# Kernel optimization log

Measured on AMD Instinct MI355X. Metric: run time of the kernel, lower is better.

Reference implementation:

```python
import jax, jax.numpy as jnp
import numpy as np
import math

D_MODEL = 1024
N_HEADS = 16
D_K = D_MODEL // N_HEADS
D_FF = 4096
B, T = 1, 4096
EPS = 1e-5


def _layer_norm(x, g, b):
    mu = jnp.mean(x, axis=-1, keepdims=True)
    var = jnp.mean(jnp.square(x - mu), axis=-1, keepdims=True)
    return (x - mu) * jax.lax.rsqrt(var + EPS) * g + b


def setup_inputs() -> dict:
    key = jax.random.key(0)
    ks = jax.random.split(key, 8)
    s = 0.02
    return {
        "x": jax.random.normal(ks[0], (B, T, D_MODEL), dtype=jnp.float32),
        "ln1_g": jnp.ones((D_MODEL,), jnp.float32),
        "ln1_b": jnp.zeros((D_MODEL,), jnp.float32),
        "w_qkv": jax.random.normal(ks[1], (3 * D_MODEL, D_MODEL), jnp.float32) * s,
        "b_qkv": jnp.zeros((3 * D_MODEL,), jnp.float32),
        "w_out": jax.random.normal(ks[2], (D_MODEL, D_MODEL), jnp.float32) * s,
        "b_out": jnp.zeros((D_MODEL,), jnp.float32),
        "ln2_g": jnp.ones((D_MODEL,), jnp.float32),
        "ln2_b": jnp.zeros((D_MODEL,), jnp.float32),
        "w1": jax.random.normal(ks[3], (D_FF, D_MODEL), jnp.float32) * s,
        "b1": jnp.zeros((D_FF,), jnp.float32),
        "w2": jax.random.normal(ks[4], (D_MODEL, D_FF), jnp.float32) * s,
        "b2": jnp.zeros((D_MODEL,), jnp.float32),
    }


def reference(x, ln1_g, ln1_b, w_qkv, b_qkv, w_out, b_out, ln2_g, ln2_b, w1, b1, w2, b2):
    Bx, Tx, C = x.shape
    # --- attention (pre-norm) ---
    h = _layer_norm(x, ln1_g, ln1_b)
    qkv = h @ w_qkv.T + b_qkv                      # [B,T,3C]
    q, k, v = jnp.split(qkv, 3, axis=-1)
    def heads(t):  # [B,T,C] -> [B,H,T,dk]
        return t.reshape(Bx, Tx, N_HEADS, D_K).transpose(0, 2, 1, 3)
    q, k, v = heads(q), heads(k), heads(v)
    scale = math.sqrt(D_K)
    scores = jnp.einsum("bhqd,bhkd->bhqk", q, k) / scale
    causal = jnp.triu(jnp.ones((Tx, Tx), dtype=bool), k=1)
    scores = jnp.where(causal[None, None], -jnp.inf, scores)
    attn_weights = jax.nn.softmax(scores, axis=-1)  # [B,H,T,T]
    out = jnp.einsum("bhqk,bhkd->bhqd", attn_weights, v)
    out = out.transpose(0, 2, 1, 3).reshape(Bx, Tx, C)
    attn_out = out @ w_out.T + b_out
    x = x + attn_out
    # --- FFN (pre-norm) ---
    h2 = _layer_norm(x, ln2_g, ln2_b)
    ff = jax.nn.gelu(h2 @ w1.T + b1, approximate=False) @ w2.T + b2
    x = x + ff
    return (x, attn_weights)
```

## Files before the change

kernel.cpp:

```cpp
#include <hip/hip_runtime.h>
#include <math.h>

typedef unsigned short u16;
typedef unsigned int u32;
typedef __attribute__((ext_vector_type(8))) short bf16x8;
typedef __attribute__((ext_vector_type(4))) float f32x4;

#define MFMA16(a, b, c) __builtin_amdgcn_mfma_f32_16x16x32_bf16((a), (b), (c), 0, 0, 0)

__device__ __forceinline__ u16 f2bf(float f) {
  u32 u = __float_as_uint(f);
  return (u16)((u + 0x7fffu + ((u >> 16) & 1u)) >> 16);
}

typedef const __attribute__((address_space(1))) u32* gas_t;
typedef __attribute__((address_space(3))) u32* las_t;
__device__ __forceinline__ void gl_lds16(const u16* g, u16* l) {
  __builtin_amdgcn_global_load_lds((gas_t)g, (las_t)l, 16, 0, 0);
}

__global__ __launch_bounds__(256) void cvt_bf16_kernel(const float* __restrict__ in,
                                                       u16* __restrict__ out, int n4) {
  int i = blockIdx.x * 256 + threadIdx.x;
  if (i >= n4) return;
  float4 v = ((const float4*)in)[i];
  ushort4 o;
  o.x = f2bf(v.x); o.y = f2bf(v.y); o.z = f2bf(v.z); o.w = f2bf(v.w);
  ((ushort4*)out)[i] = o;
}

__global__ __launch_bounds__(256) void ln_kernel(const float* __restrict__ x,
                                                 const float* __restrict__ g,
                                                 const float* __restrict__ b,
                                                 u16* __restrict__ out) {
  int row = blockIdx.x, tid = threadIdx.x;
  float4 v = ((const float4*)(x + (size_t)row * 1024))[tid];
  float s = v.x + v.y + v.z + v.w;
  float s2 = v.x * v.x + v.y * v.y + v.z * v.z + v.w * v.w;
  for (int off = 32; off; off >>= 1) { s += __shfl_xor(s, off); s2 += __shfl_xor(s2, off); }
  __shared__ float ps[4], ps2[4];
  int wave = tid >> 6;
  if ((tid & 63) == 0) { ps[wave] = s; ps2[wave] = s2; }
  __syncthreads();
  float fs = ps[0] + ps[1] + ps[2] + ps[3];
  float fs2 = ps2[0] + ps2[1] + ps2[2] + ps2[3];
  float mu = fs * (1.0f / 1024.0f);
  float var = fs2 * (1.0f / 1024.0f) - mu * mu;
  float rs = rsqrtf(var + 1e-5f);
  float4 gv = ((const float4*)g)[tid];
  float4 bv = ((const float4*)b)[tid];
  ushort4 o;
  o.x = f2bf((v.x - mu) * rs * gv.x + bv.x);
  o.y = f2bf((v.y - mu) * rs * gv.y + bv.y);
  o.z = f2bf((v.z - mu) * rs * gv.z + bv.z);
  o.w = f2bf((v.w - mu) * rs * gv.w + bv.w);
  ((ushort4*)(out + (size_t)row * 1024))[tid] = o;
}

__global__ __launch_bounds__(256) void vtrans_kernel(const u16* __restrict__ qkv,
                                                     u16* __restrict__ vt) {
  const int tt = blockIdx.x, h = blockIdx.y;
  __shared__ u16 tile[64 * 68];
  const int tid = threadIdx.x;
#pragma unroll
  for (int i = 0; i < 2; i++) {
    int c = i * 256 + tid;
    int trow = c >> 3, dc = c & 7;
    const u16* src = qkv + (size_t)(tt * 64 + trow) * 3072 + 2048 + h * 64 + dc * 8;
    uint4 v = *(const uint4*)src;
    *(uint2*)&tile[trow * 68 + dc * 8] = make_uint2(v.x, v.y);
    *(uint2*)&tile[trow * 68 + dc * 8 + 4] = make_uint2(v.z, v.w);
  }
  __syncthreads();
#pragma unroll
  for (int i = 0; i < 2; i++) {
    int c = i * 256 + tid;
    int d = c >> 3, tc = c & 7;
    ushort4 o0, o1;
    o0.x = tile[(tc * 8 + 0) * 68 + d]; o0.y = tile[(tc * 8 + 1) * 68 + d];
    o0.z = tile[(tc * 8 + 2) * 68 + d]; o0.w = tile[(tc * 8 + 3) * 68 + d];
    o1.x = tile[(tc * 8 + 4) * 68 + d]; o1.y = tile[(tc * 8 + 5) * 68 + d];
    o1.z = tile[(tc * 8 + 6) * 68 + d]; o1.w = tile[(tc * 8 + 7) * 68 + d];
    u16* dst = vt + (size_t)(h * 64 + d) * 4096 + tt * 64 + tc * 8;
    *(ushort4*)dst = o0;
    *(ushort4*)(dst + 4) = o1;
  }
}

template <int EPI>
__global__ __launch_bounds__(256, 2) void gemm_bf16(const u16* __restrict__ A,
                                                    const u16* __restrict__ B,
                                                    const float* __restrict__ bias,
                                                    const float* __restrict__ resid,
                                                    void* __restrict__ Cout,
                                                    int M, int N, int K) {
  __shared__ u16 As[128 * 32];
  __shared__ u16 Bs[128 * 32];
  const int tid = threadIdx.x, lane = tid & 63, wave = tid >> 6;
  const int wr = wave >> 1, wc = wave & 1;
  const int bm = blockIdx.y * 128, bn = blockIdx.x * 128;
  const int r = lane & 15, qd = lane >> 4;

  const u16 *ag[2], *bg[2];
  u16 *al[2], *bl[2];
#pragma unroll
  for (int i = 0; i < 2; i++) {
    int C0 = wave * 128 + i * 64;
    int sc = C0 + lane;
    int row = sc >> 2;
    int q = (sc & 3) ^ ((row >> 1) & 3);
    ag[i] = A + (size_t)(bm + row) * K + q * 8;
    al[i] = &As[C0 * 8];
    bg[i] = B + (size_t)(bn + row) * K + q * 8;
    bl[i] = &Bs[C0 * 8];
  }
  const int swz = (r >> 1) & 3;
  f32x4 acc[4][4] = {};
  for (int k0 = 0; k0 < K; k0 += 32) {
#pragma unroll
    for (int i = 0; i < 2; i++) { gl_lds16(ag[i] + k0, al[i]); gl_lds16(bg[i] + k0, bl[i]); }
    __syncthreads();
    bf16x8 af[4], bfr[4];
#pragma unroll
    for (int mi = 0; mi < 4; mi++) {
      int row = wr * 64 + mi * 16 + r;
      af[mi] = *(const bf16x8*)&As[(row * 4 + (qd ^ swz)) * 8];
    }
#pragma unroll
    for (int ni = 0; ni < 4; ni++) {
      int row = wc * 64 + ni * 16 + r;
      bfr[ni] = *(const bf16x8*)&Bs[(row * 4 + (qd ^ swz)) * 8];
    }
#pragma unroll
    for (int mi = 0; mi < 4; mi++)
#pragma unroll
      for (int ni = 0; ni < 4; ni++)
        acc[mi][ni] = MFMA16(af[mi], bfr[ni], acc[mi][ni]);
    __syncthreads();
  }
  const int crow0 = bm + wr * 64 + qd * 4;
  const int ccol0 = bn + wc * 64 + r;
#pragma unroll
  for (int ni = 0; ni < 4; ni++) {
    int col = ccol0 + ni * 16;
    float bv = bias[col];
#pragma unroll
    for (int mi = 0; mi < 4; mi++) {
#pragma unroll
      for (int rg = 0; rg < 4; rg++) {
        int row = crow0 + mi * 16 + rg;
        float v = acc[mi][ni][rg] + bv;
        if (EPI == 1) v += resid[(size_t)row * N + col];
        if (EPI == 2) v = 0.5f * v * (1.0f + erff(v * 0.70710678118654752f));
        if (EPI == 1) ((float*)Cout)[(size_t)row * N + col] = v;
        else ((u16*)Cout)[(size_t)row * N + col] = f2bf(v);
      }
    }
  }
}

__global__ __launch_bounds__(256, 2) void attn_pass1(const u16* __restrict__ qkv,
                                                     const u16* __restrict__ vt,
                                                     u16* __restrict__ aout,
                                                     float* __restrict__ mstat,
                                                     float* __restrict__ lstat) {
  const int qb = blockIdx.x, h = blockIdx.y;
  const int tid = threadIdx.x, lane = tid & 63, wave = tid >> 6;
  const int r = lane & 15, qd = lane >> 4;
  __shared__ u16 Qs[128 * 64];
  __shared__ u16 Ks[128 * 64];
  __shared__ u16 Vts[64 * 128];
  __shared__ u16 Ps[128 * 128];

#pragma unroll
  for (int i = 0; i < 4; i++) {
    int C0 = wave * 256 + i * 64;
    int sc = C0 + lane;
    int row = sc >> 3;
    int q = (sc & 7) ^ (row & 7);
    gl_lds16(qkv + (size_t)(qb * 128 + row) * 3072 + h * 64 + q * 8, &Qs[C0 * 8]);
  }
  const u16 *kg[4], *vg[4];
  u16 *kl[4], *vl[4];
#pragma unroll
  for (int i = 0; i < 4; i++) {
    int C0 = wave * 256 + i * 64;
    int sc = C0 + lane;
    int row = sc >> 3;
    int q = (sc & 7) ^ (row & 7);
    kg[i] = qkv + (size_t)row * 3072 + 1024 + h * 64 + q * 8;
    kl[i] = &Ks[C0 * 8];
    int d = sc >> 4;
    int qq = (sc & 15) ^ (d & 15);
    vg[i] = vt + (size_t)(h * 64 + d) * 4096 + qq * 8;
    vl[i] = &Vts[C0 * 8];
  }
  __syncthreads();
  bf16x8 qf[2][2];
#pragma unroll
  for (int ni = 0; ni < 2; ni++)
#pragma unroll
    for (int kk = 0; kk < 2; kk++) {
      int qrow = wave * 32 + ni * 16 + r;
      int qq = kk * 4 + qd;
      qf[ni][kk] = *(const bf16x8*)&Qs[(qrow * 8 + (qq ^ (qrow & 7))) * 8];
    }
  f32x4 ot[4][2] = {};
  float m_run[2] = {-INFINITY, -INFINITY};
  float l_run[2] = {0.f, 0.f};

  for (int kb = 0; kb <= qb; kb++) {
#pragma unroll
    for (int i = 0; i < 4; i++) {
      gl_lds16(kg[i] + (size_t)kb * 128 * 3072, kl[i]);
      gl_lds16(vg[i] + kb * 128, vl[i]);
    }
    __syncthreads();
    f32x4 st[8][2] = {};
#pragma unroll
    for (int kk = 0; kk < 2; kk++) {
      bf16x8 kf[8];
#pragma unroll
      for (int mi = 0; mi < 8; mi++) {
        int krow = mi * 16 + r;
        int qq = kk * 4 + qd;
        kf[mi] = *(const bf16x8*)&Ks[(krow * 8 + (qq ^ (krow & 7))) * 8];
      }
#pragma unroll
      for (int mi = 0; mi < 8; mi++)
#pragma unroll
        for (int ni = 0; ni < 2; ni++)
          st[mi][ni] = MFMA16(kf[mi], qf[ni][kk], st[mi][ni]);
    }
    if (kb == qb) {
#pragma unroll
      for (int mi = 0; mi < 8; mi++) {
        int k0 = mi * 16 + qd * 4;
#pragma unroll
        for (int ni = 0; ni < 2; ni++) {
          int qloc = wave * 32 + ni * 16 + r;
#pragma unroll
          for (int rg = 0; rg < 4; rg++)
            if (k0 + rg > qloc) st[mi][ni][rg] = -INFINITY;
        }
      }
    }
    float mb[2], alpha[2];
#pragma unroll
    for (int ni = 0; ni < 2; ni++) {
      float mx = -INFINITY;
#pragma unroll
      for (int mi = 0; mi < 8; mi++)
        mx = fmaxf(mx, fmaxf(fmaxf(st[mi][ni][0], st[mi][ni][1]),
                             fmaxf(st[mi][ni][2], st[mi][ni][3])));
      mx = fmaxf(mx, __shfl_xor(mx, 16));
      mx = fmaxf(mx, __shfl_xor(mx, 32));
      float mn = fmaxf(m_run[ni], mx);
      alpha[ni] = __expf((m_run[ni] - mn) * 0.125f);
      m_run[ni] = mn;
      mb[ni] = mn;
    }
#pragma unroll
    for (int ni = 0; ni < 2; ni++) {
      int qrow = wave * 32 + ni * 16 + r;
      float ls = 0.f;
#pragma unroll
      for (int mi = 0; mi < 8; mi++) {
        float p0 = __expf((st[mi][ni][0] - mb[ni]) * 0.125f);
        float p1 = __expf((st[mi][ni][1] - mb[ni]) * 0.125f);
        float p2 = __expf((st[mi][ni][2] - mb[ni]) * 0.125f);
        float p3 = __expf((st[mi][ni][3] - mb[ni]) * 0.125f);
        ls += p0 + p1 + p2 + p3;
        ushort4 pk;
        pk.x = f2bf(p0); pk.y = f2bf(p1); pk.z = f2bf(p2); pk.w = f2bf(p3);
        int qq = mi * 2 + (qd >> 1);
        int sc = qrow * 16 + (qq ^ (qrow & 15));
        *(ushort4*)&Ps[sc * 8 + (qd & 1) * 4] = pk;
      }
      ls += __shfl_xor(ls, 16);
      ls += __shfl_xor(ls, 32);
      l_run[ni] = l_run[ni] * alpha[ni] + ls;
#pragma unroll
      for (int mi = 0; mi < 4; mi++) ot[mi][ni] = ot[mi][ni] * alpha[ni];
    }
    __syncthreads();
#pragma unroll
    for (int kk = 0; kk < 4; kk++) {
      bf16x8 vf[4], pf[2];
#pragma unroll
      for (int mi = 0; mi < 4; mi++) {
        int d = mi * 16 + r;
        int qq = kk * 4 + qd;
        vf[mi] = *(const bf16x8*)&Vts[(d * 16 + (qq ^ (d & 15))) * 8];
      }
#pragma unroll
      for (int ni = 0; ni < 2; ni++) {
        int qrow = wave * 32 + ni * 16 + r;
        int qq = kk * 4 + qd;
        pf[ni] = *(const bf16x8*)&Ps[(qrow * 16 + (qq ^ (qrow & 15))) * 8];
      }
#pragma unroll
      for (int mi = 0; mi < 4; mi++)
#pragma unroll
        for (int ni = 0; ni < 2; ni++)
          ot[mi][ni] = MFMA16(vf[mi], pf[ni], ot[mi][ni]);
    }
    __syncthreads();
  }
#pragma unroll
  for (int ni = 0; ni < 2; ni++) {
    float il = 1.0f / l_run[ni];
    int qg = qb * 128 + wave * 32 + ni * 16 + r;
    if (qd == 0) {
      mstat[h * 4096 + qg] = m_run[ni];
      lstat[h * 4096 + qg] = l_run[ni];
    }
#pragma unroll
    for (int mi = 0; mi < 4; mi++) {
      ushort4 o;
      o.x = f2bf(ot[mi][ni][0] * il);
      o.y = f2bf(ot[mi][ni][1] * il);
      o.z = f2bf(ot[mi][ni][2] * il);
      o.w = f2bf(ot[mi][ni][3] * il);
      *(ushort4*)&aout[(size_t)qg * 1024 + h * 64 + mi * 16 + qd * 4] = o;
    }
  }
}

__global__ __launch_bounds__(256, 2) void attn_pass2(const u16* __restrict__ qkv,
                                                     const float* __restrict__ mstat,
                                                     const float* __restrict__ lstat,
                                                     float* __restrict__ attn) {
  const int qb = blockIdx.x, h = blockIdx.y;
  const int tid = threadIdx.x, lane = tid & 63, wave = tid >> 6;
  const int r = lane & 15, qd = lane >> 4;
  __shared__ u16 Qs[128 * 64];
  __shared__ u16 Ks[128 * 64];
#pragma unroll
  for (int i = 0; i < 4; i++) {
    int C0 = wave * 256 + i * 64;
    int sc = C0 + lane;
    int row = sc >> 3;
    int q = (sc & 7) ^ (row & 7);
    gl_lds16(qkv + (size_t)(qb * 128 + row) * 3072 + h * 64 + q * 8, &Qs[C0 * 8]);
  }
  const u16* kg[4];
  u16* kl[4];
#pragma unroll
  for (int i = 0; i < 4; i++) {
    int C0 = wave * 256 + i * 64;
    int sc = C0 + lane;
    int row = sc >> 3;
    int q = (sc & 7) ^ (row & 7);
    kg[i] = qkv + (size_t)row * 3072 + 1024 + h * 64 + q * 8;
    kl[i] = &Ks[C0 * 8];
  }
  __syncthreads();
  bf16x8 qf[2][2];
  float mrow[2], ilrow[2];
#pragma unroll
  for (int ni = 0; ni < 2; ni++) {
#pragma unroll
    for (int kk = 0; kk < 2; kk++) {
      int qrow = wave * 32 + ni * 16 + r;
      int qq = kk * 4 + qd;
      qf[ni][kk] = *(const bf16x8*)&Qs[(qrow * 8 + (qq ^ (qrow & 7))) * 8];
    }
    int qg = qb * 128 + wave * 32 + ni * 16 + r;
    mrow[ni] = mstat[h * 4096 + qg];
    ilrow[ni] = 1.0f / lstat[h * 4096 + qg];
  }
  float* ahead = attn + ((size_t)h << 24);
  for (int kb = 0; kb < 32; kb++) {
    if (kb <= qb) {
#pragma unroll
      for (int i = 0; i < 4; i++) gl_lds16(kg[i] + (size_t)kb * 128 * 3072, kl[i]);
      __syncthreads();
      f32x4 st[8][2] = {};
#pragma unroll
      for (int kk = 0; kk < 2; kk++) {
        bf16x8 kf[8];
#pragma unroll
        for (int mi = 0; mi < 8; mi++) {
          int krow = mi * 16 + r;
          int qq = kk * 4 + qd;
          kf[mi] = *(const bf16x8*)&Ks[(krow * 8 + (qq ^ (krow & 7))) * 8];
        }
#pragma unroll
        for (int mi = 0; mi < 8; mi++)
#pragma unroll
          for (int ni = 0; ni < 2; ni++)
            st[mi][ni] = MFMA16(kf[mi], qf[ni][kk], st[mi][ni]);
      }
#pragma unroll
      for (int ni = 0; ni < 2; ni++) {
        int qloc = wave * 32 + ni * 16 + r;
        size_t rowbase = (size_t)(qb * 128 + qloc) * 4096 + (size_t)kb * 128;
#pragma unroll
        for (int mi = 0; mi < 8; mi++) {
          int k0 = mi * 16 + qd * 4;
          float v0, v1, v2, v3;
          v0 = __expf((st[mi][ni][0] - mrow[ni]) * 0.125f) * ilrow[ni];
          v1 = __expf((st[mi][ni][1] - mrow[ni]) * 0.125f) * ilrow[ni];
          v2 = __expf((st[mi][ni][2] - mrow[ni]) * 0.125f) * ilrow[ni];
          v3 = __expf((st[mi][ni][3] - mrow[ni]) * 0.125f) * ilrow[ni];
          if (kb == qb) {
            if (k0 + 0 > qloc) v0 = 0.f;
            if (k0 + 1 > qloc) v1 = 0.f;
            if (k0 + 2 > qloc) v2 = 0.f;
            if (k0 + 3 > qloc) v3 = 0.f;
          }
          *(float4*)(ahead + rowbase + k0) = make_float4(v0, v1, v2, v3);
        }
      }
      __syncthreads();
    } else {
      size_t base = (size_t)(qb * 128) * 4096 + (size_t)kb * 128;
      float4 z = make_float4(0.f, 0.f, 0.f, 0.f);
#pragma unroll
      for (int i = 0; i < 16; i++) {
        int idx = i * 256 + tid;
        int ql = idx >> 5;
        int ko = (idx & 31) * 4;
        *(float4*)(ahead + base + (size_t)ql * 4096 + ko) = z;
      }
    }
  }
}

extern "C" void kernel_launch(void* const* d_in, const int* in_sizes, int n_in,
                              void* d_out, int out_size, void* d_ws, size_t ws_size,
                              hipStream_t stream) {
  const float* x     = (const float*)d_in[0];
  const float* ln1_g = (const float*)d_in[1];
  const float* ln1_b = (const float*)d_in[2];
  const float* w_qkv = (const float*)d_in[3];
  const float* b_qkv = (const float*)d_in[4];
  const float* w_out = (const float*)d_in[5];
  const float* b_out = (const float*)d_in[6];
  const float* ln2_g = (const float*)d_in[7];
  const float* ln2_b = (const float*)d_in[8];
  const float* w1    = (const float*)d_in[9];
  const float* b1    = (const float*)d_in[10];
  const float* w2    = (const float*)d_in[11];
  const float* b2    = (const float*)d_in[12];
  float* out_x = (float*)d_out;
  float* out_attn = out_x + (size_t)4096 * 1024;

  char* ws = (char*)d_ws;
  size_t off = 0;
  auto alloc = [&](size_t bytes) {
    void* p = ws + off;
    off += (bytes + 255) & ~(size_t)255;
    return p;
  };
  u16* WQKV = (u16*)alloc((size_t)3072 * 1024 * 2);
  u16* WOUT = (u16*)alloc((size_t)1024 * 1024 * 2);
  u16* W1   = (u16*)alloc((size_t)4096 * 1024 * 2);
  u16* W2   = (u16*)alloc((size_t)1024 * 4096 * 2);
  char* region = (char*)alloc((size_t)33554432);
  u16* H1  = (u16*)region;
  u16* QKV = (u16*)(region + 8388608);
  u16* FF  = (u16*)region;
  u16* VT  = (u16*)alloc((size_t)8388608);
  float* MST = (float*)alloc((size_t)262144);
  float* LST = (float*)alloc((size_t)262144);
  u16* AOUT = (u16*)alloc((size_t)8388608);
  float* X1 = (float*)alloc((size_t)16777216);
  u16* H2  = (u16*)alloc((size_t)8388608);
  (void)ws_size; (void)in_sizes; (void)n_in; (void)out_size;

  cvt_bf16_kernel<<<3072, 256, 0, stream>>>(w_qkv, WQKV, 786432);
  cvt_bf16_kernel<<<1024, 256, 0, stream>>>(w_out, WOUT, 262144);
  cvt_bf16_kernel<<<4096, 256, 0, stream>>>(w1, W1, 1048576);
  cvt_bf16_kernel<<<4096, 256, 0, stream>>>(w2, W2, 1048576);
  ln_kernel<<<4096, 256, 0, stream>>>(x, ln1_g, ln1_b, H1);
  gemm_bf16<0><<<dim3(24, 32), 256, 0, stream>>>(H1, WQKV, b_qkv, nullptr, QKV, 4096, 3072, 1024);
  vtrans_kernel<<<dim3(64, 16), 256, 0, stream>>>(QKV, VT);
  attn_pass1<<<dim3(32, 16), 256, 0, stream>>>(QKV, VT, AOUT, MST, LST);
  gemm_bf16<1><<<dim3(8, 32), 256, 0, stream>>>(AOUT, WOUT, b_out, x, X1, 4096, 1024, 1024);
  attn_pass2<<<dim3(32, 16), 256, 0, stream>>>(QKV, MST, LST, out_attn);
  ln_kernel<<<4096, 256, 0, stream>>>(X1, ln2_g, ln2_b, H2);
  gemm_bf16<2><<<dim3(32, 32), 256, 0, stream>>>(H2, W1, b1, nullptr, FF, 4096, 4096, 1024);
  gemm_bf16<1><<<dim3(8, 32), 256, 0, stream>>>(FF, W2, b2, X1, out_x, 4096, 1024, 4096);
}
```

Measured before the change: 1.595 ms.

## Fuse FF2 GEMM with attention-weights pass into one interleaved launch

```diff
diff --git a/kernel.cpp b/kernel.cpp
--- a/kernel.cpp
+++ b/kernel.cpp
@@ -19,14 +19,22 @@
   __builtin_amdgcn_global_load_lds((gas_t)g, (las_t)l, 16, 0, 0);
 }
 
-__global__ __launch_bounds__(256) void cvt_bf16_kernel(const float* __restrict__ in,
-                                                       u16* __restrict__ out, int n4) {
-  int i = blockIdx.x * 256 + threadIdx.x;
-  if (i >= n4) return;
-  float4 v = ((const float4*)in)[i];
+__global__ __launch_bounds__(256) void cvt_all_kernel(const float* __restrict__ s0, u16* __restrict__ d0,
+                                                      const float* __restrict__ s1, u16* __restrict__ d1,
+                                                      const float* __restrict__ s2, u16* __restrict__ d2,
+                                                      const float* __restrict__ s3, u16* __restrict__ d3) {
+  int blk = blockIdx.x, t = threadIdx.x;
+  const float* src;
+  u16* dst;
+  int i;
+  if (blk < 3072)      { src = s0; dst = d0; i = blk * 256 + t; }
+  else if (blk < 4096) { src = s1; dst = d1; i = (blk - 3072) * 256 + t; }
+  else if (blk < 8192) { src = s2; dst = d2; i = (blk - 4096) * 256 + t; }
+  else                 { src = s3; dst = d3; i = (blk - 8192) * 256 + t; }
+  float4 v = ((const float4*)src)[i];
   ushort4 o;
   o.x = f2bf(v.x); o.y = f2bf(v.y); o.z = f2bf(v.z); o.w = f2bf(v.w);
-  ((ushort4*)out)[i] = o;
+  ((ushort4*)dst)[i] = o;
 }
 
 __global__ __launch_bounds__(256) void ln_kernel(const float* __restrict__ x,
@@ -88,18 +96,16 @@
 }
 
 template <int EPI>
-__global__ __launch_bounds__(256, 2) void gemm_bf16(const u16* __restrict__ A,
-                                                    const u16* __restrict__ B,
-                                                    const float* __restrict__ bias,
-                                                    const float* __restrict__ resid,
-                                                    void* __restrict__ Cout,
-                                                    int M, int N, int K) {
-  __shared__ u16 As[128 * 32];
-  __shared__ u16 Bs[128 * 32];
+__device__ __forceinline__ void gemm_body(const u16* __restrict__ A, const u16* __restrict__ B,
+                                          const float* __restrict__ bias,
+                                          const float* __restrict__ resid,
+                                          void* __restrict__ Cout, int M, int N, int K,
+                                          int bxi, int byi, u16* As, u16* Bs) {
   const int tid = threadIdx.x, lane = tid & 63, wave = tid >> 6;
   const int wr = wave >> 1, wc = wave & 1;
-  const int bm = blockIdx.y * 128, bn = blockIdx.x * 128;
+  const int bm = byi * 128, bn = bxi * 128;
   const int r = lane & 15, qd = lane >> 4;
+  (void)M;
 
   const u16 *ag[2], *bg[2];
   u16 *al[2], *bl[2];
@@ -157,6 +163,18 @@
       }
     }
   }
+}
+
+template <int EPI>
+__global__ __launch_bounds__(256, 2) void gemm_bf16(const u16* __restrict__ A,
+                                                    const u16* __restrict__ B,
+                                                    const float* __restrict__ bias,
+                                                    const float* __restrict__ resid,
+                                                    void* __restrict__ Cout,
+                                                    int M, int N, int K) {
+  __shared__ u16 As[128 * 32];
+  __shared__ u16 Bs[128 * 32];
+  gemm_body<EPI>(A, B, bias, resid, Cout, M, N, K, blockIdx.x, blockIdx.y, As, Bs);
 }
 
 __global__ __launch_bounds__(256, 2) void attn_pass1(const u16* __restrict__ qkv,
@@ -327,15 +345,13 @@
   }
 }
 
-__global__ __launch_bounds__(256, 2) void attn_pass2(const u16* __restrict__ qkv,
-                                                     const float* __restrict__ mstat,
-                                                     const float* __restrict__ lstat,
-                                                     float* __restrict__ attn) {
-  const int qb = blockIdx.x, h = blockIdx.y;
+__device__ __forceinline__ void pass2_body(const u16* __restrict__ qkv,
+                                           const float* __restrict__ mstat,
+                                           const float* __restrict__ lstat,
+                                           float* __restrict__ attn, int qb, int h,
+                                           u16* Qs, u16* Ks) {
   const int tid = threadIdx.x, lane = tid & 63, wave = tid >> 6;
   const int r = lane & 15, qd = lane >> 4;
-  __shared__ u16 Qs[128 * 64];
-  __shared__ u16 Ks[128 * 64];
 #pragma unroll
   for (int i = 0; i < 4; i++) {
     int C0 = wave * 256 + i * 64;
@@ -425,6 +441,23 @@
         *(float4*)(ahead + base + (size_t)ql * 4096 + ko) = z;
       }
     }
+  }
+}
+
+__global__ __launch_bounds__(256, 2) void ff2_pass2_fused(
+    const u16* __restrict__ A, const u16* __restrict__ B, const float* __restrict__ bias,
+    const float* __restrict__ resid, float* __restrict__ Cout,
+    const u16* __restrict__ qkv, const float* __restrict__ mstat,
+    const float* __restrict__ lstat, float* __restrict__ attn) {
+  __shared__ u16 smem[128 * 64 * 2];
+  int idx = blockIdx.x;
+  int q3 = idx / 3, r3 = idx - q3 * 3;
+  if (r3 == 0) {
+    gemm_body<1>(A, B, bias, resid, (void*)Cout, 4096, 1024, 4096, q3 & 7, q3 >> 3,
+                 smem, smem + 128 * 32);
+  } else {
+    int p = q3 * 2 + (r3 - 1);
+    pass2_body(qkv, mstat, lstat, attn, p & 31, p >> 5, smem, smem + 128 * 64);
   }
 }
 
@@ -458,11 +491,10 @@
   u16* WOUT = (u16*)alloc((size_t)1024 * 1024 * 2);
   u16* W1   = (u16*)alloc((size_t)4096 * 1024 * 2);
   u16* W2   = (u16*)alloc((size_t)1024 * 4096 * 2);
-  char* region = (char*)alloc((size_t)33554432);
-  u16* H1  = (u16*)region;
-  u16* QKV = (u16*)(region + 8388608);
-  u16* FF  = (u16*)region;
-  u16* VT  = (u16*)alloc((size_t)8388608);
+  u16* H1   = (u16*)alloc((size_t)8388608);
+  u16* QKV  = (u16*)alloc((size_t)25165824);
+  u16* FF   = (u16*)alloc((size_t)33554432);
+  u16* VT   = (u16*)alloc((size_t)8388608);
   float* MST = (float*)alloc((size_t)262144);
   float* LST = (float*)alloc((size_t)262144);
   u16* AOUT = (u16*)alloc((size_t)8388608);
@@ -470,17 +502,13 @@
   u16* H2  = (u16*)alloc((size_t)8388608);
   (void)ws_size; (void)in_sizes; (void)n_in; (void)out_size;
 
-  cvt_bf16_kernel<<<3072, 256, 0, stream>>>(w_qkv, WQKV, 786432);
-  cvt_bf16_kernel<<<1024, 256, 0, stream>>>(w_out, WOUT, 262144);
-  cvt_bf16_kernel<<<4096, 256, 0, stream>>>(w1, W1, 1048576);
-  cvt_bf16_kernel<<<4096, 256, 0, stream>>>(w2, W2, 1048576);
+  cvt_all_kernel<<<12288, 256, 0, stream>>>(w_qkv, WQKV, w_out, WOUT, w1, W1, w2, W2);
   ln_kernel<<<4096, 256, 0, stream>>>(x, ln1_g, ln1_b, H1);
   gemm_bf16<0><<<dim3(24, 32), 256, 0, stream>>>(H1, WQKV, b_qkv, nullptr, QKV, 4096, 3072, 1024);
   vtrans_kernel<<<dim3(64, 16), 256, 0, stream>>>(QKV, VT);
   attn_pass1<<<dim3(32, 16), 256, 0, stream>>>(QKV, VT, AOUT, MST, LST);
   gemm_bf16<1><<<dim3(8, 32), 256, 0, stream>>>(AOUT, WOUT, b_out, x, X1, 4096, 1024, 1024);
-  attn_pass2<<<dim3(32, 16), 256, 0, stream>>>(QKV, MST, LST, out_attn);
   ln_kernel<<<4096, 256, 0, stream>>>(X1, ln2_g, ln2_b, H2);
   gemm_bf16<2><<<dim3(32, 32), 256, 0, stream>>>(H2, W1, b1, nullptr, FF, 4096, 4096, 1024);
-  gemm_bf16<1><<<dim3(8, 32), 256, 0, stream>>>(FF, W2, b2, X1, out_x, 4096, 1024, 4096);
-}
+  ff2_pass2_fused<<<768, 256, 0, stream>>>(FF, W2, b2, X1, out_x, QKV, MST, LST, out_attn);
+}
```

Result: faster. 1.547 ms (-3.0%).
